# Performance work log

Measured on AMD Instinct MI355X. Metric: run time of the kernel, lower is better.

Reference implementation:

```python
import jax, jax.numpy as jnp
import numpy as np

K = 16            # neighbors
RATIO = 0.25      # sampling ratio -> M = N*RATIO
EPS = 1e-5        # BatchNorm eps


def _fps(pts, m):
    # Farthest point sampling for one cloud. pts: (N,3) -> (m,) int32 indices.
    n = pts.shape[0]

    def body(carry, _):
        dist, last = carry                      # dist: (N,) min sq-dist to selected set
        d = jnp.sum((pts - pts[last]) ** 2, axis=-1)
        dist = jnp.minimum(dist, d)
        nxt = jnp.argmax(dist).astype(jnp.int32)
        return (dist, nxt), nxt

    init = (jnp.full((n,), jnp.inf, pts.dtype), jnp.int32(0))
    _, rest = jax.lax.scan(body, init, None, length=m - 1)
    return jnp.concatenate([jnp.zeros((1,), jnp.int32), rest])


def setup_inputs() -> dict:
    key = jax.random.key(0)
    ks = jax.random.split(key, 3)
    B, N, C_IN, C_OUT = 8, 8192, 64, 128
    x = jax.random.normal(ks[0], (B, N, C_IN), jnp.float32)
    p = jax.random.normal(ks[1], (B, N, 3), jnp.float32)
    W = jax.random.normal(ks[2], (C_OUT, C_IN), jnp.float32) * 0.05
    gamma = jnp.ones((C_OUT,), jnp.float32)
    beta = jnp.zeros((C_OUT,), jnp.float32)
    run_mean = jnp.zeros((C_OUT,), jnp.float32)
    run_var = jnp.ones((C_OUT,), jnp.float32)
    return {"x": x, "p": p, "W": W, "gamma": gamma, "beta": beta,
            "run_mean": run_mean, "run_var": run_var}


def reference(x, p, W, gamma, beta, run_mean, run_var):
    B, N, _ = x.shape
    M = int(N * RATIO)

    # 1) FPS sample M points per cloud
    idx_fps = jax.vmap(lambda q: _fps(q, M))(p)                   # (B, M)
    p_out = jnp.take_along_axis(p, idx_fps[..., None], axis=1)    # (B, M, 3)

    # 2) KNN: squared distances (B, M, N), sorted K nearest via top_k on -dist
    d2 = (jnp.sum(p_out ** 2, -1)[..., None]
          + jnp.sum(p ** 2, -1)[:, None, :]
          - 2.0 * jnp.einsum('bmd,bnd->bmn', p_out, p))
    _, nbr = jax.lax.top_k(-d2, K)                                # (B, M, K) ascending dist

    # 3) Pointwise MLP: Conv1d(k=1, no bias) == matmul, then BN (eval) + ReLU
    h = jnp.einsum('bnc,oc->bno', x, W)                           # (B, N, C_OUT)
    h = (h - run_mean) * jax.lax.rsqrt(run_var + EPS) * gamma + beta
    h = jax.nn.relu(h)

    # 4) Gather neighbor features and max-pool over K
    flat = nbr.reshape(B, M * K)
    feats = jnp.take_along_axis(h, flat[..., None], axis=1).reshape(B, M, K, -1)
    y = jnp.max(feats, axis=2)                                    # (B, M, C_OUT)
    return y, p_out
```

## Files before the change

kernel.cpp:

```cpp
#include <hip/hip_runtime.h>

#define B_   8
#define N_   8192
#define CIN  64
#define COUT 128
#define M_   2048
#define K_   16

typedef float v2f __attribute__((ext_vector_type(2)));

template <int CTRL>
__device__ __forceinline__ unsigned long long dpp64(unsigned long long x) {
  int lo = (int)(unsigned)(x & 0xFFFFFFFFull);
  int hi = (int)(unsigned)(x >> 32);
  int dlo = __builtin_amdgcn_update_dpp(lo, lo, CTRL, 0xF, 0xF, false);
  int dhi = __builtin_amdgcn_update_dpp(hi, hi, CTRL, 0xF, 0xF, false);
  return ((unsigned long long)(unsigned)dhi << 32) | (unsigned)dlo;
}

__device__ __forceinline__ unsigned long long readlane_u64(unsigned long long k, int l) {
  unsigned lo = (unsigned)__builtin_amdgcn_readlane((int)(unsigned)(k & 0xFFFFFFFFull), l);
  unsigned hi = (unsigned)__builtin_amdgcn_readlane((int)(unsigned)(k >> 32), l);
  return ((unsigned long long)hi << 32) | lo;
}

__device__ __forceinline__ unsigned long long wave_max_u64(unsigned long long k) {
  unsigned long long t;
  t = dpp64<0x111>(k); k = t > k ? t : k;
  t = dpp64<0x112>(k); k = t > k ? t : k;
  t = dpp64<0x114>(k); k = t > k ? t : k;
  t = dpp64<0x118>(k); k = t > k ? t : k;
  t = dpp64<0x142>(k); k = t > k ? t : k;
  t = dpp64<0x143>(k); k = t > k ? t : k;
  return readlane_u64(k, 63);
}

__device__ __forceinline__ unsigned long long wave_min_u64(unsigned long long k) {
  unsigned long long t;
  t = dpp64<0x111>(k); k = t < k ? t : k;
  t = dpp64<0x112>(k); k = t < k ? t : k;
  t = dpp64<0x114>(k); k = t < k ? t : k;
  t = dpp64<0x118>(k); k = t < k ? t : k;
  t = dpp64<0x142>(k); k = t < k ? t : k;
  t = dpp64<0x143>(k); k = t < k ? t : k;
  return readlane_u64(k, 63);
}

#define FTH 512
#define FPT 16
#define MROWS2 32

__global__ __launch_bounds__(512) void fps_mlp_kernel(
    const float* __restrict__ p, float* __restrict__ p_out,
    const float* __restrict__ x, const float* __restrict__ W,
    const float* __restrict__ gamma, const float* __restrict__ beta,
    const float* __restrict__ rmean, const float* __restrict__ rvar,
    float* __restrict__ h) {
#pragma clang fp contract(off)
  __shared__ __align__(16) unsigned char smem[139776];

  const int tid = threadIdx.x;

  if (blockIdx.x >= 8) {
    float* wt = (float*)smem;
    float* xs = (float*)(smem + 33792);

    const int o  = tid & 127;
    const int rg = tid >> 7;
    const int rowBase = (blockIdx.x - 8) * MROWS2;

    for (int idx = tid; idx < COUT * CIN; idx += 512) {
      const int oo = idx >> 6, cc = idx & 63;
      wt[cc * 132 + oo] = W[idx];
    }
    ((float4*)xs)[tid] = ((const float4*)(x + (size_t)rowBase * CIN))[tid];
    __syncthreads();

    float acc[8] = {0.f, 0.f, 0.f, 0.f, 0.f, 0.f, 0.f, 0.f};
#pragma unroll
    for (int c4 = 0; c4 < CIN / 4; c4++) {
      const float w0 = wt[(4 * c4 + 0) * 132 + o];
      const float w1 = wt[(4 * c4 + 1) * 132 + o];
      const float w2 = wt[(4 * c4 + 2) * 132 + o];
      const float w3 = wt[(4 * c4 + 3) * 132 + o];
#pragma unroll
      for (int i = 0; i < 8; i++) {
        const float4 xv = *(const float4*)&xs[(rg * 8 + i) * CIN + c4 * 4];
        acc[i] += xv.x * w0 + xv.y * w1 + xv.z * w2 + xv.w * w3;
      }
    }
    const float mu = rmean[o];
    const float sc = rsqrtf(rvar[o] + 1e-5f) * gamma[o];
    const float bt = beta[o];
#pragma unroll
    for (int i = 0; i < 8; i++) {
      const float v = (acc[i] - mu) * sc + bt;
      h[(size_t)(rowBase + rg * 8 + i) * COUT + o] = fmaxf(v, 0.f);
    }
    return;
  }

  float4* pc4 = (float4*)smem;
  unsigned long long (*wred)[8] =
      (unsigned long long (*)[8])(smem + 131072);
  int* idxHist = (int*)(smem + 131072 + 128);

  const int b  = blockIdx.x;
  const int wv = tid >> 6;
  const int ln = tid & 63;

  const float* pb = p + (size_t)b * N_ * 3;
  for (int n = tid; n < N_; n += FTH)
    pc4[n] = make_float4(pb[3 * n + 0], pb[3 * n + 1], pb[3 * n + 2], 0.f);
  if (tid == 0) idxHist[0] = 0;
  __syncthreads();

  float4 c0 = pc4[0];
  float cx = c0.x, cy = c0.y, cz = c0.z;

  v2f X2[8], Y2[8], Z2[8], D2[8];
#pragma unroll
  for (int j = 0; j < 8; j++) {
    float4 a = pc4[tid + (2 * j) * FTH];
    float4 c = pc4[tid + (2 * j + 1) * FTH];
    X2[j] = (v2f){a.x, c.x};
    Y2[j] = (v2f){a.y, c.y};
    Z2[j] = (v2f){a.z, c.z};
    D2[j] = (v2f){__builtin_inff(), __builtin_inff()};
  }

  int buf = 0;
  for (int it = 1; it < M_; ++it) {
    const v2f cxv = {cx, cx}, cyv = {cy, cy}, czv = {cz, cz};
    float bd = -1.0f; int bk = 0;
#pragma unroll
    for (int j = 0; j < 8; j++) {
      v2f dx = X2[j] - cxv;
      v2f dy = Y2[j] - cyv;
      v2f dz = Z2[j] - czv;
      v2f m1 = dx * dx;
      v2f m2 = dy * dy;
      v2f s  = m1 + m2;
      v2f m3 = dz * dz;
      v2f d  = s + m3;
      v2f dm = __builtin_elementwise_min(D2[j], d);
      D2[j] = dm;
      if (dm.x > bd) { bd = dm.x; bk = 2 * j; }
      if (dm.y > bd) { bd = dm.y; bk = 2 * j + 1; }
    }
    const int n = tid + (bk << 9);
    unsigned long long key =
        ((unsigned long long)__float_as_uint(bd) << 32) |
        (unsigned)(N_ - 1 - n);
    key = wave_max_u64(key);
    if (ln == 0) wred[buf][wv] = key;
    __syncthreads();
    unsigned long long kk = wred[buf][ln & 7];
    unsigned long long t;
    t = dpp64<0x111>(kk); kk = t > kk ? t : kk;
    t = dpp64<0x112>(kk); kk = t > kk ? t : kk;
    t = dpp64<0x114>(kk); kk = t > kk ? t : kk;
    const unsigned long long m = readlane_u64(kk, 7);
    const int nw = N_ - 1 - (int)(unsigned)(m & 0xFFFFFFFFu);
    float4 cc = pc4[nw];
    cx = cc.x; cy = cc.y; cz = cc.z;
    if (tid == 0) idxHist[it] = nw;
    buf ^= 1;
  }
  __syncthreads();

  float* po = p_out + (size_t)b * M_ * 3;
  for (int mi = tid; mi < M_; mi += FTH) {
    float4 v = pc4[idxHist[mi]];
    po[mi * 3 + 0] = v.x;
    po[mi * 3 + 1] = v.y;
    po[mi * 3 + 2] = v.z;
  }
}

#define UMAXK 0xFFFFFFFFFFFFFFFFull
#define QPB  16

__global__ __launch_bounds__(1024) void knn_kernel(
    const float* __restrict__ p, const float* __restrict__ p_out,
    const float* __restrict__ h, float* __restrict__ y) {
#pragma clang fp contract(off)
  __shared__ float4 pc4[N_];
  __shared__ int winLds[QPB][K_];

  const int t    = threadIdx.x;
  const int wv   = t >> 6;
  const int lane = t & 63;
  const int b    = blockIdx.x & 7;
  const int grp  = blockIdx.x >> 3;
  const int q    = b * M_ + grp * QPB + wv;

  const float* pb = p + (size_t)b * N_ * 3;
  for (int n = t; n < N_; n += 1024) {
    float xx = pb[3 * n + 0], yy = pb[3 * n + 1], zz = pb[3 * n + 2];
    float sn = (xx * xx + yy * yy) + zz * zz;
    pc4[n] = make_float4(xx, yy, zz, sn);
  }
  __syncthreads();

  const float qx = p_out[q * 3 + 0];
  const float qy = p_out[q * 3 + 1];
  const float qz = p_out[q * 3 + 2];
  const float sq = (qx * qx + qy * qy) + qz * qz;

  unsigned long long c0 = UMAXK, c1 = UMAXK, c2 = UMAXK, c3 = UMAXK;
#pragma unroll 4
  for (int j = 0; j < 128; j++) {
    const int n = lane + (j << 6);
    float4 v = pc4[n];
    float dot = __builtin_fmaf(qz, v.z,
                __builtin_fmaf(qy, v.y, qx * v.x));
    float d2 = (sq + v.w) - 2.0f * dot;
    unsigned u = __float_as_uint(d2);
    u ^= (unsigned)((int)u >> 31) | 0x80000000u;
    unsigned long long key = ((unsigned long long)u << 32) | (unsigned)n;
    if (key < c3) {
      unsigned long long x2 = key, mn;
      mn = x2 < c0 ? x2 : c0; x2 = x2 < c0 ? c0 : x2; c0 = mn;
      mn = x2 < c1 ? x2 : c1; x2 = x2 < c1 ? c1 : x2; c1 = mn;
      mn = x2 < c2 ? x2 : c2; x2 = x2 < c2 ? c2 : x2; c2 = mn;
      c3 = x2 < c3 ? x2 : c3;
    }
  }

  int count = 4;
  unsigned long long em0 = 0ull, em1 = 0ull;
  unsigned long long mykey = UMAXK;

  for (int k = 0; k < K_; k++) {
    unsigned long long cnd = (count > 0) ? c0 : UMAXK;
    unsigned long long win = wave_min_u64(cnd);
    if (lane == k) mykey = win;
    const int nstar = (int)(unsigned)(win & 0xFFFFFFFFu);
    if ((nstar & 63) == lane) {
      const int j = nstar >> 6;
      if (j < 64) em0 |= 1ull << j; else em1 |= 1ull << (j - 64);
      c0 = c1; c1 = c2; c2 = c3; c3 = UMAXK; count--;
      if (count == 0 && k < K_ - 1) {
        c0 = c1 = c2 = c3 = UMAXK;
        for (int j2 = 0; j2 < 128; j2++) {
          bool ex = (j2 < 64) ? ((em0 >> j2) & 1ull) : ((em1 >> (j2 - 64)) & 1ull);
          if (!ex) {
            const int n2 = lane + (j2 << 6);
            float4 v = pc4[n2];
            float dot = __builtin_fmaf(qz, v.z,
                        __builtin_fmaf(qy, v.y, qx * v.x));
            float d2 = (sq + v.w) - 2.0f * dot;
            unsigned u = __float_as_uint(d2);
            u ^= (unsigned)((int)u >> 31) | 0x80000000u;
            unsigned long long kk2 = ((unsigned long long)u << 32) | (unsigned)n2;
            if (kk2 < c3) {
              unsigned long long x2 = kk2, mn;
              mn = x2 < c0 ? x2 : c0; x2 = x2 < c0 ? c0 : x2; c0 = mn;
              mn = x2 < c1 ? x2 : c1; x2 = x2 < c1 ? c1 : x2; c1 = mn;
              mn = x2 < c2 ? x2 : c2; x2 = x2 < c2 ? c2 : x2; c2 = mn;
              c3 = x2 < c3 ? x2 : c3;
            }
          }
        }
        count = 4;
      }
    }
  }

  if (lane < K_) winLds[wv][lane] = (int)(unsigned)(mykey & 0xFFFFFFFFu);
  __syncthreads();

  const float* hb = h + (size_t)b * N_ * COUT;
  float2 acc = make_float2(-__builtin_inff(), -__builtin_inff());
#pragma unroll
  for (int i = 0; i < K_; i++) {
    const int n = winLds[wv][i];
    float2 v = *(const float2*)(hb + (size_t)n * COUT + lane * 2);
    acc.x = fmaxf(acc.x, v.x);
    acc.y = fmaxf(acc.y, v.y);
  }
  *(float2*)(y + (size_t)q * COUT + lane * 2) = acc;
}

extern "C" void kernel_launch(void* const* d_in, const int* in_sizes, int n_in,
                              void* d_out, int out_size, void* d_ws, size_t ws_size,
                              hipStream_t stream) {
  const float* x     = (const float*)d_in[0];
  const float* p     = (const float*)d_in[1];
  const float* W     = (const float*)d_in[2];
  const float* gamma = (const float*)d_in[3];
  const float* beta  = (const float*)d_in[4];
  const float* rmean = (const float*)d_in[5];
  const float* rvar  = (const float*)d_in[6];

  float* y     = (float*)d_out;
  float* p_out = y + (size_t)B_ * M_ * COUT;
  float* h     = (float*)d_ws;

  fps_mlp_kernel<<<8 + (B_ * N_) / MROWS2, 512, 0, stream>>>(
      p, p_out, x, W, gamma, beta, rmean, rvar, h);
  knn_kernel<<<B_ * (M_ / QPB), 1024, 0, stream>>>(p, p_out, h, y);
}
```

Baseline: 2.117 ms.

## Publish FPS chunks and MLP rows via flags so KNN can start early

FPS blocks now write p_out in 256-row chunks during the loop and set per-chunk release flags. MLP blocks set per-tile done flags, and the KNN kernel spin-waits on these flags instead of relying purely on kernel ordering. The FPS distance computation is also fused into FMAs, and the argmax update is made branchless. Because both kernels are launched on the same stream, the flag-based overlap cannot actually run the two concurrently. The flags are never reset between calls, and the FMA contraction changes rounding relative to the reference.

After: 2.190 ms. 1.03x slower.

```diff
diff --git a/kernel.cpp b/kernel.cpp
--- a/kernel.cpp
+++ b/kernel.cpp
@@ -6,6 +6,8 @@
 #define COUT 128
 #define M_   2048
 #define K_   16
+
+#define MAGIC 0x5AFEC0DEu
 
 typedef float v2f __attribute__((ext_vector_type(2)));
 
@@ -55,7 +57,8 @@
     const float* __restrict__ x, const float* __restrict__ W,
     const float* __restrict__ gamma, const float* __restrict__ beta,
     const float* __restrict__ rmean, const float* __restrict__ rvar,
-    float* __restrict__ h) {
+    float* __restrict__ h, unsigned* __restrict__ fpsFlags,
+    unsigned* __restrict__ mlpDone, int publish) {
 #pragma clang fp contract(off)
   __shared__ __align__(16) unsigned char smem[139776];
 
@@ -67,7 +70,8 @@
 
     const int o  = tid & 127;
     const int rg = tid >> 7;
-    const int rowBase = (blockIdx.x - 8) * MROWS2;
+    const int bid = blockIdx.x - 8;
+    const int rowBase = bid * MROWS2;
 
     for (int idx = tid; idx < COUT * CIN; idx += 512) {
       const int oo = idx >> 6, cc = idx & 63;
@@ -97,6 +101,10 @@
       const float v = (acc[i] - mu) * sc + bt;
       h[(size_t)(rowBase + rg * 8 + i) * COUT + o] = fmaxf(v, 0.f);
     }
+    __syncthreads();
+    if (publish && tid == 0)
+      __hip_atomic_store(&mlpDone[bid], MAGIC, __ATOMIC_RELEASE,
+                         __HIP_MEMORY_SCOPE_AGENT);
     return;
   }
 
@@ -117,6 +125,7 @@
 
   float4 c0 = pc4[0];
   float cx = c0.x, cy = c0.y, cz = c0.z;
+  float* po = p_out + (size_t)b * M_ * 3;
 
   v2f X2[8], Y2[8], Z2[8], D2[8];
 #pragma unroll
@@ -138,15 +147,16 @@
       v2f dx = X2[j] - cxv;
       v2f dy = Y2[j] - cyv;
       v2f dz = Z2[j] - czv;
-      v2f m1 = dx * dx;
-      v2f m2 = dy * dy;
-      v2f s  = m1 + m2;
-      v2f m3 = dz * dz;
-      v2f d  = s + m3;
+      v2f d  = __builtin_elementwise_fma(dz, dz,
+               __builtin_elementwise_fma(dy, dy, dx * dx));
       v2f dm = __builtin_elementwise_min(D2[j], d);
       D2[j] = dm;
-      if (dm.x > bd) { bd = dm.x; bk = 2 * j; }
-      if (dm.y > bd) { bd = dm.y; bk = 2 * j + 1; }
+      bool gx = dm.x > bd;
+      bk = gx ? (2 * j) : bk;
+      bd = gx ? dm.x : bd;
+      bool gy = dm.y > bd;
+      bk = gy ? (2 * j + 1) : bk;
+      bd = gy ? dm.y : bd;
     }
     const int n = tid + (bk << 9);
     unsigned long long key =
@@ -155,6 +165,21 @@
     key = wave_max_u64(key);
     if (ln == 0) wred[buf][wv] = key;
     __syncthreads();
+
+    if (publish) {
+      if ((it & 255) == 0 && tid < 256) {
+        const int row = ((it >> 8) - 1 << 8) + tid;
+        float4 v = pc4[idxHist[row]];
+        float* pr = po + (size_t)row * 3;
+        pr[0] = v.x; pr[1] = v.y; pr[2] = v.z;
+      }
+      if ((it & 255) == 1 && it > 256 && tid == 0) {
+        const int c = ((it - 1) >> 8) - 1;
+        __hip_atomic_store(&fpsFlags[b * 8 + c], MAGIC, __ATOMIC_RELEASE,
+                           __HIP_MEMORY_SCOPE_AGENT);
+      }
+    }
+
     unsigned long long kk = wred[buf][ln & 7];
     unsigned long long t;
     t = dpp64<0x111>(kk); kk = t > kk ? t : kk;
@@ -169,12 +194,24 @@
   }
   __syncthreads();
 
-  float* po = p_out + (size_t)b * M_ * 3;
-  for (int mi = tid; mi < M_; mi += FTH) {
-    float4 v = pc4[idxHist[mi]];
-    po[mi * 3 + 0] = v.x;
-    po[mi * 3 + 1] = v.y;
-    po[mi * 3 + 2] = v.z;
+  if (publish) {
+    if (tid < 256) {
+      const int row = 1792 + tid;
+      float4 v = pc4[idxHist[row]];
+      float* pr = po + (size_t)row * 3;
+      pr[0] = v.x; pr[1] = v.y; pr[2] = v.z;
+    }
+    __syncthreads();
+    if (tid == 0)
+      __hip_atomic_store(&fpsFlags[b * 8 + 7], MAGIC, __ATOMIC_RELEASE,
+                         __HIP_MEMORY_SCOPE_AGENT);
+  } else {
+    for (int mi = tid; mi < M_; mi += FTH) {
+      float4 v = pc4[idxHist[mi]];
+      po[mi * 3 + 0] = v.x;
+      po[mi * 3 + 1] = v.y;
+      po[mi * 3 + 2] = v.z;
+    }
   }
 }
 
@@ -183,7 +220,9 @@
 
 __global__ __launch_bounds__(1024) void knn_kernel(
     const float* __restrict__ p, const float* __restrict__ p_out,
-    const float* __restrict__ h, float* __restrict__ y) {
+    const float* __restrict__ h, float* __restrict__ y,
+    const unsigned* __restrict__ fpsFlags,
+    const unsigned* __restrict__ mlpDone, int wait) {
 #pragma clang fp contract(off)
   __shared__ float4 pc4[N_];
   __shared__ int winLds[QPB][K_];
@@ -200,6 +239,15 @@
     float xx = pb[3 * n + 0], yy = pb[3 * n + 1], zz = pb[3 * n + 2];
     float sn = (xx * xx + yy * yy) + zz * zz;
     pc4[n] = make_float4(xx, yy, zz, sn);
+  }
+
+  if (wait && t == 0) {
+    const int chunk = grp >> 4;
+    int guard = 0;
+    while (__hip_atomic_load(&fpsFlags[b * 8 + chunk], __ATOMIC_ACQUIRE,
+                             __HIP_MEMORY_SCOPE_AGENT) != MAGIC &&
+           ++guard < (1 << 23))
+      __builtin_amdgcn_s_sleep(2);
   }
   __syncthreads();
 
@@ -269,6 +317,14 @@
   }
 
   if (lane < K_) winLds[wv][lane] = (int)(unsigned)(mykey & 0xFFFFFFFFu);
+
+  if (wait && t < 256) {
+    int guard = 0;
+    while (__hip_atomic_load(&mlpDone[b * 256 + t], __ATOMIC_ACQUIRE,
+                             __HIP_MEMORY_SCOPE_AGENT) != MAGIC &&
+           ++guard < (1 << 23))
+      __builtin_amdgcn_s_sleep(2);
+  }
   __syncthreads();
 
   const float* hb = h + (size_t)b * N_ * COUT;
@@ -298,7 +354,13 @@
   float* p_out = y + (size_t)B_ * M_ * COUT;
   float* h     = (float*)d_ws;
 
+  const size_t hBytes = (size_t)B_ * N_ * COUT * 4;
+  const int overlap = (ws_size >= hBytes + 16384) ? 1 : 0;
+  unsigned* fpsFlags = (unsigned*)((char*)d_ws + hBytes);
+  unsigned* mlpDone  = fpsFlags + 64;
+
   fps_mlp_kernel<<<8 + (B_ * N_) / MROWS2, 512, 0, stream>>>(
-      p, p_out, x, W, gamma, beta, rmean, rvar, h);
-  knn_kernel<<<B_ * (M_ / QPB), 1024, 0, stream>>>(p, p_out, h, y);
-}
+      p, p_out, x, W, gamma, beta, rmean, rvar, h, fpsFlags, mlpDone, overlap);
+  knn_kernel<<<B_ * (M_ / QPB), 1024, 0, stream>>>(
+      p, p_out, h, y, fpsFlags, mlpDone, overlap);
+}
```
